# Performance work log

Measured on AMD Instinct MI355X. Metric: run time of the kernel, lower is better.

Reference implementation:

```python
import jax, jax.numpy as jnp
import numpy as np
from jax import lax

SIM_RATIO = 0.5
TAU = 1e-4
BN_EPS = 1e-5
COS_EPS = 1e-6
LEAKY_SLOPE = 0.01


def setup_inputs() -> dict:
    key = jax.random.key(0)
    ks = jax.random.split(key, 4)
    B, N, D = 2048, 50000, 128
    user_item_id = jax.random.randint(ks[0], (B, 2), 0, N, dtype=jnp.int64 if jax.config.jax_enable_x64 else jnp.int32).astype(jnp.int32)
    item_feature = jax.random.normal(ks[1], (B, 2 * D), dtype=jnp.float32)
    all_items = jax.random.normal(ks[2], (N, D), dtype=jnp.float32)
    # Linear(2D -> D) params (stored transposed: x @ W + b), BatchNorm1d affine params
    W = jax.random.normal(ks[3], (2 * D, D), dtype=jnp.float32) / np.float32(np.sqrt(2 * D))
    b = jnp.zeros((D,), jnp.float32)
    gamma = jnp.ones((D,), jnp.float32)
    beta = jnp.zeros((D,), jnp.float32)
    return {"user_item_id": user_item_id, "item_feature": item_feature,
            "all_items": all_items, "W": W, "b": b, "gamma": gamma, "beta": beta}


def _mlp(x, W, b, gamma, beta):
    # Linear + BatchNorm1d (training mode: batch stats, biased var) + LeakyReLU
    h = x @ W + b                                  # [B, D]
    mean = h.mean(axis=0)
    var = ((h - mean) ** 2).mean(axis=0)
    h = (h - mean) * lax.rsqrt(var + BN_EPS) * gamma + beta
    return jnp.where(h >= 0, h, LEAKY_SLOPE * h)


def reference(user_item_id, item_feature, all_items, W, b, gamma, beta):
    B = item_feature.shape[0]
    N = all_items.shape[0]
    h = _mlp(item_feature, W, b, gamma, beta)       # [B, D]
    scores = h @ all_items.T                         # [B, N]
    # hard gumbel-softmax, tau=1e-4
    g = jax.random.gumbel(jax.random.key(42), scores.shape, scores.dtype)
    soft = jax.nn.softmax((scores + g) / TAU, axis=-1)
    idx = jnp.argmax(soft, axis=-1)                  # [B]
    onehot = jax.nn.one_hot(idx, N, dtype=scores.dtype)
    probs = onehot + soft - lax.stop_gradient(soft)  # straight-through hard one-hot
    repl_feat = probs @ all_items                    # [B, D] (one-hot gather via matmul)
    repl_items = (jnp.arange(N, dtype=scores.dtype) * probs).sum(axis=1).astype(jnp.int32)
    orig_feat = all_items[user_item_id[:, 1]]        # [B, D]
    # cosine similarity along dim=1 with eps=1e-6 (torch semantics)
    dot = (orig_feat * repl_feat).sum(axis=1)
    n1 = jnp.maximum(jnp.linalg.norm(orig_feat, axis=1), COS_EPS)
    n2 = jnp.maximum(jnp.linalg.norm(repl_feat, axis=1), COS_EPS)
    sim = dot / (n1 * n2)
    sim = (sim + 1.0) / 2.0                          # regularize_similarity
    labels = jnp.full((B,), SIM_RATIO, dtype=sim.dtype)
    sim_loss = jnp.mean((sim - labels) ** 2)         # SimilarityMarginLoss ~ MSE to ratio
    return repl_items, sim_loss, sim.mean()
```

## Files before the change

### kernel.cpp

```cpp
#include <hip/hip_runtime.h>
#include <math.h>

#define TINYF 1.17549435e-38f
#define GMAX 16.0f
#define NT16 3125
#define SPT16 49

typedef __attribute__((ext_vector_type(8))) short bf16x8;
typedef __attribute__((ext_vector_type(4))) float f32x4;

__device__ __forceinline__ unsigned rotl32(unsigned x, int r) {
  return (x << r) | (x >> (32 - r));
}

__device__ __forceinline__ unsigned tf2x32_xor(unsigned x0, unsigned x1) {
  const unsigned k0 = 0u, k1 = 42u, k2 = 0x1BD11BF0u;
  x0 += k0; x1 += k1;
#define TFR(r) { x0 += x1; x1 = rotl32(x1, r); x1 ^= x0; }
  TFR(13) TFR(15) TFR(26) TFR(6)
  x0 += k1; x1 += k2 + 1u;
  TFR(17) TFR(29) TFR(16) TFR(24)
  x0 += k2; x1 += k0 + 2u;
  TFR(13) TFR(15) TFR(26) TFR(6)
  x0 += k0; x1 += k1 + 3u;
  TFR(17) TFR(29) TFR(16) TFR(24)
  x0 += k1; x1 += k2 + 4u;
  TFR(13) TFR(15) TFR(26) TFR(6)
  x0 += k2; x1 += k0 + 5u;
#undef TFR
  return x0 ^ x1;
}

__device__ __forceinline__ float gumbel_from_bits(unsigned bits) {
  float f = __uint_as_float((bits >> 9) | 0x3f800000u) - 1.0f;
  float u = fmaxf(f, TINYF);
  return -logf(-logf(u));
}

__device__ __forceinline__ unsigned ordf(float v) {
  unsigned b = __float_as_uint(v);
  return (b & 0x80000000u) ? ~b : (b | 0x80000000u);
}
__device__ __forceinline__ float unordf(unsigned u) {
  unsigned b = (u & 0x80000000u) ? (u & 0x7FFFFFFFu) : ~u;
  return __uint_as_float(b);
}

__device__ __forceinline__ unsigned short f2bf(float f) {
  unsigned u = __float_as_uint(f);
  unsigned r = u + 0x7FFFu + ((u >> 16) & 1u);
  return (unsigned short)(r >> 16);
}
__device__ __forceinline__ unsigned pk2(float a, float b) {
  return (unsigned)f2bf(a) | ((unsigned)f2bf(b) << 16);
}
__device__ __forceinline__ int bswz(int b) { return b ^ (((b >> 8) & 7) << 4); }

__device__ __attribute__((noinline)) void resolve_cand(
    int R, int J, float s, float ERRC,
    const float* __restrict__ hfin, const float* __restrict__ items,
    const unsigned* __restrict__ V0u,
    unsigned long long* __restrict__ rowslot, const volatile unsigned* hiw) {
  const unsigned v0 = V0u[R];
  const unsigned hi0 = hiw[2 * R + 1];
  float tv = v0 ? unordf(v0) : -3.4e38f;
  if (hi0) tv = fmaxf(tv, unordf(hi0));
  const float thr2 = tv - ERRC;
  const float d = thr2 - s;
  const unsigned bits = tf2x32_xor(0u, (unsigned)R * 50000u + (unsigned)J);
  const float f = __uint_as_float((bits >> 9) | 0x3f800000u) - 1.0f;
  const float u = fmaxf(f, TINYF);
  const float thr_u = __expf(-__expf(-d)) * (1.0f - 2e-5f);
  if (u < thr_u) return;
  const float g = -logf(-logf(u));
  if (s + g < thr2) return;
  const float4* hp = (const float4*)(hfin + (size_t)R * 128);
  const float4* ap = (const float4*)(items + (size_t)J * 128);
  float4 a4 = {0.f, 0.f, 0.f, 0.f};
#pragma unroll
  for (int k = 0; k < 32; ++k) {
    float4 h = hp[k];
    float4 b = ap[k];
    a4.x = fmaf(h.x, b.x, a4.x);
    a4.y = fmaf(h.y, b.y, a4.y);
    a4.z = fmaf(h.z, b.z, a4.z);
    a4.w = fmaf(h.w, b.w, a4.w);
  }
  const float v = ((a4.x + a4.y) + (a4.z + a4.w)) + g;
  const unsigned ov = ordf(v);
  if (ov >= hiw[2 * R + 1]) {
    const unsigned long long pk =
        ((unsigned long long)ov << 32) | (0xFFFFFFFFu - (unsigned)J);
    atomicMax(&rowslot[R], pk);
  }
}

__global__ void k_hraw(const float* __restrict__ x, const float* __restrict__ W,
                       const float* __restrict__ b, float* __restrict__ hraw,
                       unsigned long long* __restrict__ rowslot,
                       unsigned* __restrict__ V0u, float* __restrict__ norms) {
  __shared__ float sx[256];
  const int i = blockIdx.x;
  const int d = threadIdx.x;
  if (d == 0) {
    rowslot[i] = 0ull;
    V0u[i] = 0u;
    if (i == 0) { norms[0] = 0.0f; norms[1] = 0.0f; }
  }
  sx[d] = x[i * 256 + d];
  sx[d + 128] = x[i * 256 + 128 + d];
  __syncthreads();
  double acc = 0.0;
  for (int k = 0; k < 256; ++k)
    acc = fma((double)sx[k], (double)W[k * 128 + d], acc);
  hraw[i * 128 + d] = (float)acc + b[d];
}

__global__ void k_bca(const float* __restrict__ items,
                      unsigned short* __restrict__ ib,
                      float* __restrict__ norms) {
  __shared__ float red[4];
  const int t = threadIdx.x;
  const int row = blockIdx.x * 32 + (t >> 3);
  const int rc = row > 49999 ? 49999 : row;
  const int c = (t & 7) * 16;
  const float4* p = (const float4*)(items + (size_t)rc * 128 + c);
  const float4 v0 = p[0], v1 = p[1], v2 = p[2], v3 = p[3];
  float ss = v0.x * v0.x + v0.y * v0.y + v0.z * v0.z + v0.w * v0.w +
             v1.x * v1.x + v1.y * v1.y + v1.z * v1.z + v1.w * v1.w +
             v2.x * v2.x + v2.y * v2.y + v2.z * v2.z + v2.w * v2.w +
             v3.x * v3.x + v3.y * v3.y + v3.z * v3.z + v3.w * v3.w;
  if (row <= 49999) {
    uint4 o0, o1;
    o0.x = pk2(v0.x, v0.y); o0.y = pk2(v0.z, v0.w);
    o0.z = pk2(v1.x, v1.y); o0.w = pk2(v1.z, v1.w);
    o1.x = pk2(v2.x, v2.y); o1.y = pk2(v2.z, v2.w);
    o1.z = pk2(v3.x, v3.y); o1.w = pk2(v3.z, v3.w);
    uint4* dst = (uint4*)(ib + (size_t)row * 128 + c);
    dst[0] = o0; dst[1] = o1;
  }
  ss += __shfl_xor(ss, 1);
  ss += __shfl_xor(ss, 2);
  ss += __shfl_xor(ss, 4);
  ss = fmaxf(ss, __shfl_xor(ss, 8));
  ss = fmaxf(ss, __shfl_xor(ss, 16));
  ss = fmaxf(ss, __shfl_xor(ss, 32));
  if ((t & 63) == 0) red[t >> 6] = ss;
  __syncthreads();
  if (t == 0) {
    float mx = fmaxf(fmaxf(red[0], red[1]), fmaxf(red[2], red[3]));
    atomicMax((unsigned*)&norms[1], __float_as_uint(mx));
  }
}

__global__ void k_bnstats(const float* __restrict__ hraw,
                          float* __restrict__ meanv, float* __restrict__ rsv) {
  __shared__ double red[256];
  const int d = blockIdx.x;
  const int t = threadIdx.x;
  double s = 0.0;
  for (int i = t; i < 2048; i += 256) s += (double)hraw[i * 128 + d];
  red[t] = s;
  __syncthreads();
  for (int off = 128; off > 0; off >>= 1) {
    if (t < off) red[t] += red[t + off];
    __syncthreads();
  }
  const float m = (float)(red[0] * (1.0 / 2048.0));
  __syncthreads();
  double v = 0.0;
  for (int i = t; i < 2048; i += 256) {
    float dd = __fsub_rn(hraw[i * 128 + d], m);
    v += (double)dd * (double)dd;
  }
  red[t] = v;
  __syncthreads();
  for (int off = 128; off > 0; off >>= 1) {
    if (t < off) red[t] += red[t + off];
    __syncthreads();
  }
  if (t == 0) {
    float var = (float)(red[0] * (1.0 / 2048.0));
    float vpe = __fadd_rn(var, 1e-5f);
    meanv[d] = m;
    rsv[d] = (float)(1.0 / sqrt((double)vpe));
  }
}

__global__ void k_apply(const float* __restrict__ hraw,
                        const float* __restrict__ meanv, const float* __restrict__ rsv,
                        const float* __restrict__ gamma, const float* __restrict__ beta,
                        float* __restrict__ hfin, unsigned short* __restrict__ hb,
                        float* __restrict__ norms) {
  __shared__ float red[256];
  const int t = threadIdx.x;
  const int idx = blockIdx.x * 256 + t;
  const int d = idx & 127;
  float h = hraw[idx];
  float hn = __fadd_rn(__fmul_rn(__fmul_rn(__fsub_rn(h, meanv[d]), rsv[d]), gamma[d]), beta[d]);
  float o = (hn >= 0.0f) ? hn : __fmul_rn(0.01f, hn);
  hfin[idx] = o;
  hb[idx] = f2bf(o);
  red[t] = o * o;
  __syncthreads();
  for (int off = 64; off > 0; off >>= 1) {
    if ((t & 127) < off) red[t] += red[t + off];
    __syncthreads();
  }
  if ((t & 127) == 0) atomicMax((unsigned*)&norms[0], __float_as_uint(red[t]));
}

__global__ __launch_bounds__(256, 2) void k_seed(
    const unsigned short* __restrict__ hb, const unsigned short* __restrict__ ib,
    const float* __restrict__ norms, unsigned* __restrict__ V0u) {
  const int t = threadIdx.x;
  const int w = t >> 6, l = t & 63;
  const int lg = l >> 4, lr = l & 15;
  const int rg = blockIdx.x >> 3;
  const int jspan = blockIdx.x & 7;
  const int r0w = rg * 64 + w * 16;
  const float ERRC = 0.004f * sqrtf(norms[0] * norms[1]) + 0.01f;

  const unsigned short* aB0 = hb + (size_t)(r0w + lr) * 128 + lg * 8;
  bf16x8 Afrag[4];
#pragma unroll
  for (int kb = 0; kb < 4; ++kb) Afrag[kb] = *(const bf16x8*)(aB0 + kb * 32);

  float vmax[4] = {-3.4e38f, -3.4e38f, -3.4e38f, -3.4e38f};
  for (int itr = 0; itr < 8; ++itr) {
    const int J = jspan * 128 + itr * 16 + lr;
    const unsigned short* bp = ib + (size_t)J * 128 + lg * 8;
    f32x4 acc = (f32x4){0.f, 0.f, 0.f, 0.f};
#pragma unroll
    for (int kb = 0; kb < 4; ++kb)
      acc = __builtin_amdgcn_mfma_f32_16x16x32_bf16(Afrag[kb], *(const bf16x8*)(bp + kb * 32), acc, 0, 0, 0);
#pragma unroll
    for (int q = 0; q < 4; ++q) {
      const int R = r0w + lg * 4 + q;
      const float g = gumbel_from_bits(tf2x32_xor(0u, (unsigned)R * 50000u + (unsigned)J));
      vmax[q] = fmaxf(vmax[q], acc[q] + g);
    }
  }
#pragma unroll
  for (int m = 1; m <= 8; m <<= 1)
#pragma unroll
    for (int q = 0; q < 4; ++q) vmax[q] = fmaxf(vmax[q], __shfl_xor(vmax[q], m));
  if (lr == 0) {
#pragma unroll
    for (int q = 0; q < 4; ++q)
      atomicMax(&V0u[r0w + lg * 4 + q], ordf(vmax[q] - ERRC));
  }
}

__global__ __launch_bounds__(256, 2) void k_screen(
    const unsigned short* __restrict__ hb, const float* __restrict__ hfin,
    const float* __restrict__ items, const unsigned short* __restrict__ ib,
    const unsigned* __restrict__ V0u,
    const float* __restrict__ norms, unsigned long long* __restrict__ rowslot) {
  __shared__ __align__(16) unsigned short Bs[4][2][16 * 128];
  __shared__ unsigned qk[4][128];
  __shared__ float qsh[4][128];

  const int t = threadIdx.x;
  const int w = t >> 6, l = t & 63;
  const int lg = l >> 4, lr = l & 15;
  const int rg = blockIdx.x >> 6;
  const int span = blockIdx.x & 63;
  const int r0w = rg * 64 + w * 16;
  const int tile0 = span * SPT16;
  int nt = NT16 - tile0;
  nt = nt < 0 ? 0 : (nt > SPT16 ? SPT16 : nt);
  if (nt == 0) return;

  const float ERRC = 0.004f * sqrtf(norms[0] * norms[1]) + 0.01f;
  const volatile unsigned* hiw = (const volatile unsigned*)rowslot;

  const unsigned short* aB0 = hb + (size_t)(r0w + lr) * 128 + lg * 8;
  bf16x8 Afrag[4];
#pragma unroll
  for (int kb = 0; kb < 4; ++kb) Afrag[kb] = *(const bf16x8*)(aB0 + kb * 32);

  char* wlds = (char*)Bs + w * 8192;
  const char* ibc = (const char*)ib;
  int so[4];
#pragma unroll
  for (int c = 0; c < 4; ++c) {
    const int row = c * 4 + (l >> 4);
    const int col = (l & 15) * 16;
    so[c] = row * 256 + (col ^ ((row & 7) << 4));
  }

#define ISSUE(tl, pbuf)                                                        \
  {                                                                            \
    const char* gs = ibc + (size_t)(tl) * 4096;                                \
    char* ld = wlds + (pbuf) * 4096;                                           \
    __builtin_amdgcn_global_load_lds((const unsigned*)(gs + so[0]),            \
                                     (unsigned*)(ld), 16, 0, 0);               \
    __builtin_amdgcn_global_load_lds((const unsigned*)(gs + so[1]),            \
                                     (unsigned*)(ld + 1024), 16, 0, 0);        \
    __builtin_amdgcn_global_load_lds((const unsigned*)(gs + so[2]),            \
                                     (unsigned*)(ld + 2048), 16, 0, 0);        \
    __builtin_amdgcn_global_load_lds((const unsigned*)(gs + so[3]),            \
                                     (unsigned*)(ld + 3072), 16, 0, 0);        \
  }
#define WAITVM4() { asm volatile("s_waitcnt vmcnt(4)" ::: "memory"); \
                    __builtin_amdgcn_sched_barrier(0); }
#define WAITVM0() { asm volatile("s_waitcnt vmcnt(0)" ::: "memory"); \
                    __builtin_amdgcn_sched_barrier(0); }

  ISSUE(tile0, 0)

  const unsigned long long lml = (1ull << l) - 1ull;
  unsigned qn = 0;
  float th1[4];

  int pb = 0;
  for (int it = 0; it < nt; ++it) {
    const int j0 = (tile0 + it) * 16;

    if (it + 1 < nt) {
      ISSUE(tile0 + it + 1, pb ^ 1)
      WAITVM4()
    } else {
      WAITVM0()
    }

    if ((it & 7) == 0) {
      float tvl = -3.4e38f;
      if (l < 16) {
        const int R = r0w + l;
        const unsigned v0 = V0u[R];
        if (v0) tvl = unordf(v0);
        const unsigned hi = hiw[2 * R + 1];
        if (hi) tvl = fmaxf(tvl, unordf(hi));
      }
#pragma unroll
      for (int q = 0; q < 4; ++q)
        th1[q] = __shfl(tvl, lg * 4 + q) - GMAX - ERRC;
    }

    f32x4 a0 = (f32x4){0.f, 0.f, 0.f, 0.f};
    f32x4 a1 = (f32x4){0.f, 0.f, 0.f, 0.f};
    const char* tb = wlds + pb * 4096;
    {
      bf16x8 b0 = *(const bf16x8*)(tb + bswz(lr * 256 + 0 * 64 + lg * 16));
      bf16x8 b1 = *(const bf16x8*)(tb + bswz(lr * 256 + 1 * 64 + lg * 16));
      bf16x8 b2 = *(const bf16x8*)(tb + bswz(lr * 256 + 2 * 64 + lg * 16));
      bf16x8 b3 = *(const bf16x8*)(tb + bswz(lr * 256 + 3 * 64 + lg * 16));
      a0 = __builtin_amdgcn_mfma_f32_16x16x32_bf16(Afrag[0], b0, a0, 0, 0, 0);
      a1 = __builtin_amdgcn_mfma_f32_16x16x32_bf16(Afrag[1], b1, a1, 0, 0, 0);
      a0 = __builtin_amdgcn_mfma_f32_16x16x32_bf16(Afrag[2], b2, a0, 0, 0, 0);
      a1 = __builtin_amdgcn_mfma_f32_16x16x32_bf16(Afrag[3], b3, a1, 0, 0, 0);
    }
    const f32x4 acc = a0 + a1;

#pragma unroll
    for (int q = 0; q < 4; ++q) {
      const float s = acc[q];
      const int J = j0 + lr;
      const bool c = (s >= th1[q]);
      const unsigned long long m = __ballot(c);
      if (m) {
        if (c) {
          const unsigned idx = qn + (unsigned)__popcll(m & lml);
          qk[w][idx] = ((unsigned)(lg * 4 + q) << 16) | (unsigned)J;
          qsh[w][idx] = s;
        }
        qn += (unsigned)__popcll(m);
        if (qn >= 64) {
          for (unsigned i = (unsigned)l; i < qn; i += 64) {
            const unsigned key = qk[w][i];
            resolve_cand(r0w + (int)(key >> 16), (int)(key & 0xFFFFu),
                         qsh[w][i], ERRC, hfin, items, V0u, rowslot, hiw);
          }
          qn = 0;
        }
      }
    }

    pb ^= 1;
  }

  for (unsigned i = (unsigned)l; i < qn; i += 64) {
    const unsigned key = qk[w][i];
    resolve_cand(r0w + (int)(key >> 16), (int)(key & 0xFFFFu),
                 qsh[w][i], ERRC, hfin, items, V0u, rowslot, hiw);
  }
#undef ISSUE
#undef WAITVM4
#undef WAITVM0
}

__global__ void k_final(const unsigned long long* __restrict__ rowslot,
                        const int* __restrict__ uid, const float* __restrict__ items,
                        float* __restrict__ dout, float* __restrict__ simv) {
  const int r = blockIdx.x;
  const int lane = threadIdx.x;
  const unsigned long long pk = rowslot[r];
  const int bi = (int)(0xFFFFFFFFu - (unsigned)pk);
  if (lane == 0) dout[r] = (float)bi;

  const int orig = uid[r * 2 + 1];
  float o1 = items[(size_t)orig * 128 + lane];
  float o2 = items[(size_t)orig * 128 + 64 + lane];
  float p1 = items[(size_t)bi * 128 + lane];
  float p2 = items[(size_t)bi * 128 + 64 + lane];
  float d = o1 * p1 + o2 * p2;
  float s1 = o1 * o1 + o2 * o2;
  float s2 = p1 * p1 + p2 * p2;
  for (int off = 32; off > 0; off >>= 1) {
    d += __shfl_down(d, off);
    s1 += __shfl_down(s1, off);
    s2 += __shfl_down(s2, off);
  }
  if (lane == 0) {
    float n1 = fmaxf(sqrtf(s1), 1e-6f);
    float n2 = fmaxf(sqrtf(s2), 1e-6f);
    float sim = d / (n1 * n2);
    simv[r] = (sim + 1.0f) * 0.5f;
  }
}

__global__ void k_reduce(const float* __restrict__ simv, float* __restrict__ dout) {
  __shared__ double rl[256];
  __shared__ double rs[256];
  const int t = threadIdx.x;
  double L = 0.0, S = 0.0;
  for (int i = t; i < 2048; i += 256) {
    double s = (double)simv[i];
    double dd = s - 0.5;
    L += dd * dd;
    S += s;
  }
  rl[t] = L; rs[t] = S;
  __syncthreads();
  for (int off = 128; off > 0; off >>= 1) {
    if (t < off) { rl[t] += rl[t + off]; rs[t] += rs[t + off]; }
    __syncthreads();
  }
  if (t == 0) {
    dout[2048] = (float)(rl[0] * (1.0 / 2048.0));
    dout[2049] = (float)(rs[0] * (1.0 / 2048.0));
  }
}

extern "C" void kernel_launch(void* const* d_in, const int* in_sizes, int n_in,
                              void* d_out, int out_size, void* d_ws, size_t ws_size,
                              hipStream_t stream) {
  const int* uid = (const int*)d_in[0];
  const float* xfeat = (const float*)d_in[1];
  const float* items = (const float*)d_in[2];
  const float* W = (const float*)d_in[3];
  const float* bias = (const float*)d_in[4];
  const float* gamma = (const float*)d_in[5];
  const float* beta = (const float*)d_in[6];

  float* ws = (float*)d_ws;
  float* hraw = ws;
  float* hfin = ws + 262144;
  float* meanv = ws + 524288;
  float* rsv = ws + 524416;
  unsigned* V0u = (unsigned*)(ws + 524544);
  float* simv = ws + 526592;
  float* norms = ws + 528640;
  unsigned long long* rowslot =
      (unsigned long long*)(ws + 528642);
  unsigned short* hb = (unsigned short*)(ws + 532740);
  unsigned short* ib = (unsigned short*)(ws + 663812);
  float* dout = (float*)d_out;

  hipLaunchKernelGGL(k_hraw, dim3(2048), dim3(128), 0, stream, xfeat, W, bias, hraw, rowslot, V0u, norms);
  hipLaunchKernelGGL(k_bca, dim3(1563), dim3(256), 0, stream, items, ib, norms);
  hipLaunchKernelGGL(k_bnstats, dim3(128), dim3(256), 0, stream, hraw, meanv, rsv);
  hipLaunchKernelGGL(k_apply, dim3(1024), dim3(256), 0, stream, hraw, meanv, rsv, gamma, beta, hfin, hb, norms);
  hipLaunchKernelGGL(k_seed, dim3(256), dim3(256), 0, stream, hb, ib, norms, V0u);
  hipLaunchKernelGGL(k_screen, dim3(2048), dim3(256), 0, stream, hb, hfin, items, ib, V0u, norms, rowslot);
  hipLaunchKernelGGL(k_final, dim3(2048), dim3(64), 0, stream, rowslot, uid, items, dout, simv);
  hipLaunchKernelGGL(k_reduce, dim3(1), dim3(256), 0, stream, simv, dout);
}
```

Measured before the change: 356.4 us.

## Process two row tiles per wave in screen kernel and fuse pre-kernels

Each wave in the screening kernel now covers 32 rows (two 16-row A fragments) instead of 16. Every loaded B tile of item embeddings feeds twice as many MFMAs, which halves the grid and the repeated item-tile traffic. The hraw linear and bf16 conversion kernels are merged into a single launch, and the per-row init is replaced with memsets. The trade-off is higher register pressure from the doubled fragments and accumulators, and fewer blocks to balance the screening work.

```diff
diff --git a/kernel.cpp b/kernel.cpp
--- a/kernel.cpp
+++ b/kernel.cpp
@@ -95,61 +95,56 @@
   }
 }
 
-__global__ void k_hraw(const float* __restrict__ x, const float* __restrict__ W,
-                       const float* __restrict__ b, float* __restrict__ hraw,
-                       unsigned long long* __restrict__ rowslot,
-                       unsigned* __restrict__ V0u, float* __restrict__ norms) {
-  __shared__ float sx[256];
-  const int i = blockIdx.x;
-  const int d = threadIdx.x;
-  if (d == 0) {
-    rowslot[i] = 0ull;
-    V0u[i] = 0u;
-    if (i == 0) { norms[0] = 0.0f; norms[1] = 0.0f; }
-  }
-  sx[d] = x[i * 256 + d];
-  sx[d + 128] = x[i * 256 + 128 + d];
-  __syncthreads();
-  double acc = 0.0;
-  for (int k = 0; k < 256; ++k)
-    acc = fma((double)sx[k], (double)W[k * 128 + d], acc);
-  hraw[i * 128 + d] = (float)acc + b[d];
-}
-
-__global__ void k_bca(const float* __restrict__ items,
-                      unsigned short* __restrict__ ib,
-                      float* __restrict__ norms) {
+__global__ void k_pre(const float* __restrict__ x, const float* __restrict__ W,
+                      const float* __restrict__ b, float* __restrict__ hraw,
+                      const float* __restrict__ items,
+                      unsigned short* __restrict__ ib, float* __restrict__ norms) {
+  __shared__ float sx[2][256];
   __shared__ float red[4];
   const int t = threadIdx.x;
-  const int row = blockIdx.x * 32 + (t >> 3);
-  const int rc = row > 49999 ? 49999 : row;
-  const int c = (t & 7) * 16;
-  const float4* p = (const float4*)(items + (size_t)rc * 128 + c);
-  const float4 v0 = p[0], v1 = p[1], v2 = p[2], v3 = p[3];
-  float ss = v0.x * v0.x + v0.y * v0.y + v0.z * v0.z + v0.w * v0.w +
-             v1.x * v1.x + v1.y * v1.y + v1.z * v1.z + v1.w * v1.w +
-             v2.x * v2.x + v2.y * v2.y + v2.z * v2.z + v2.w * v2.w +
-             v3.x * v3.x + v3.y * v3.y + v3.z * v3.z + v3.w * v3.w;
-  if (row <= 49999) {
-    uint4 o0, o1;
-    o0.x = pk2(v0.x, v0.y); o0.y = pk2(v0.z, v0.w);
-    o0.z = pk2(v1.x, v1.y); o0.w = pk2(v1.z, v1.w);
-    o1.x = pk2(v2.x, v2.y); o1.y = pk2(v2.z, v2.w);
-    o1.z = pk2(v3.x, v3.y); o1.w = pk2(v3.z, v3.w);
-    uint4* dst = (uint4*)(ib + (size_t)row * 128 + c);
-    dst[0] = o0; dst[1] = o1;
-  }
-  ss += __shfl_xor(ss, 1);
-  ss += __shfl_xor(ss, 2);
-  ss += __shfl_xor(ss, 4);
-  ss = fmaxf(ss, __shfl_xor(ss, 8));
-  ss = fmaxf(ss, __shfl_xor(ss, 16));
-  ss = fmaxf(ss, __shfl_xor(ss, 32));
-  if ((t & 63) == 0) red[t >> 6] = ss;
-  __syncthreads();
-  if (t == 0) {
-    float mx = fmaxf(fmaxf(red[0], red[1]), fmaxf(red[2], red[3]));
-    atomicMax((unsigned*)&norms[1], __float_as_uint(mx));
+  const int bid = blockIdx.x;
+  if (bid < 1024) {
+    const int rr = t >> 7, d = t & 127;
+    const int i = bid * 2 + rr;
+    sx[rr][d] = x[i * 256 + d];
+    sx[rr][d + 128] = x[i * 256 + 128 + d];
+    __syncthreads();
+    double acc = 0.0;
+    for (int k = 0; k < 256; ++k)
+      acc = fma((double)sx[rr][k], (double)W[k * 128 + d], acc);
+    hraw[i * 128 + d] = (float)acc + b[d];
+  } else {
+    const int bb = bid - 1024;
+    const int row = bb * 32 + (t >> 3);
+    const int rc = row > 49999 ? 49999 : row;
+    const int c = (t & 7) * 16;
+    const float4* p = (const float4*)(items + (size_t)rc * 128 + c);
+    const float4 v0 = p[0], v1 = p[1], v2 = p[2], v3 = p[3];
+    float ss = v0.x * v0.x + v0.y * v0.y + v0.z * v0.z + v0.w * v0.w +
+               v1.x * v1.x + v1.y * v1.y + v1.z * v1.z + v1.w * v1.w +
+               v2.x * v2.x + v2.y * v2.y + v2.z * v2.z + v2.w * v2.w +
+               v3.x * v3.x + v3.y * v3.y + v3.z * v3.z + v3.w * v3.w;
+    if (row <= 49999) {
+      uint4 o0, o1;
+      o0.x = pk2(v0.x, v0.y); o0.y = pk2(v0.z, v0.w);
+      o0.z = pk2(v1.x, v1.y); o0.w = pk2(v1.z, v1.w);
+      o1.x = pk2(v2.x, v2.y); o1.y = pk2(v2.z, v2.w);
+      o1.z = pk2(v3.x, v3.y); o1.w = pk2(v3.z, v3.w);
+      uint4* dst = (uint4*)(ib + (size_t)row * 128 + c);
+      dst[0] = o0; dst[1] = o1;
+    }
+    ss += __shfl_xor(ss, 1);
+    ss += __shfl_xor(ss, 2);
+    ss += __shfl_xor(ss, 4);
+    ss = fmaxf(ss, __shfl_xor(ss, 8));
+    ss = fmaxf(ss, __shfl_xor(ss, 16));
+    ss = fmaxf(ss, __shfl_xor(ss, 32));
+    if ((t & 63) == 0) red[t >> 6] = ss;
+    __syncthreads();
+    if (t == 0) {
+      float mx = fmaxf(fmaxf(red[0], red[1]), fmaxf(red[2], red[3]));
+      atomicMax((unsigned*)&norms[1], __float_as_uint(mx));
+    }
   }
 }
 
@@ -266,7 +261,7 @@
   const int lg = l >> 4, lr = l & 15;
   const int rg = blockIdx.x >> 6;
   const int span = blockIdx.x & 63;
-  const int r0w = rg * 64 + w * 16;
+  const int r0w = rg * 128 + w * 32;
   const int tile0 = span * SPT16;
   int nt = NT16 - tile0;
   nt = nt < 0 ? 0 : (nt > SPT16 ? SPT16 : nt);
@@ -276,9 +271,12 @@
   const volatile unsigned* hiw = (const volatile unsigned*)rowslot;
 
   const unsigned short* aB0 = hb + (size_t)(r0w + lr) * 128 + lg * 8;
-  bf16x8 Afrag[4];
-#pragma unroll
-  for (int kb = 0; kb < 4; ++kb) Afrag[kb] = *(const bf16x8*)(aB0 + kb * 32);
+  bf16x8 Afrag[2][4];
+#pragma unroll
+  for (int kb = 0; kb < 4; ++kb) {
+    Afrag[0][kb] = *(const bf16x8*)(aB0 + kb * 32);
+    Afrag[1][kb] = *(const bf16x8*)(aB0 + 16 * 128 + kb * 32);
+  }
 
   char* wlds = (char*)Bs + w * 8192;
   const char* ibc = (const char*)ib;
@@ -312,7 +310,7 @@
 
   const unsigned long long lml = (1ull << l) - 1ull;
   unsigned qn = 0;
-  float th1[4];
+  float th1[2][4];
 
   int pb = 0;
   for (int it = 0; it < nt; ++it) {
@@ -327,7 +325,7 @@
 
     if ((it & 7) == 0) {
       float tvl = -3.4e38f;
-      if (l < 16) {
+      if (l < 32) {
         const int R = r0w + l;
         const unsigned v0 = V0u[R];
         if (v0) tvl = unordf(v0);
@@ -335,48 +333,59 @@
         if (hi) tvl = fmaxf(tvl, unordf(hi));
       }
 #pragma unroll
-      for (int q = 0; q < 4; ++q)
-        th1[q] = __shfl(tvl, lg * 4 + q) - GMAX - ERRC;
-    }
-
-    f32x4 a0 = (f32x4){0.f, 0.f, 0.f, 0.f};
-    f32x4 a1 = (f32x4){0.f, 0.f, 0.f, 0.f};
+      for (int rt = 0; rt < 2; ++rt)
+#pragma unroll
+        for (int q = 0; q < 4; ++q)
+          th1[rt][q] = __shfl(tvl, rt * 16 + lg * 4 + q) - GMAX - ERRC;
+    }
+
+    f32x4 p0 = (f32x4){0.f, 0.f, 0.f, 0.f};
+    f32x4 p1 = (f32x4){0.f, 0.f, 0.f, 0.f};
+    f32x4 q0 = (f32x4){0.f, 0.f, 0.f, 0.f};
+    f32x4 q1 = (f32x4){0.f, 0.f, 0.f, 0.f};
     const char* tb = wlds + pb * 4096;
     {
       bf16x8 b0 = *(const bf16x8*)(tb + bswz(lr * 256 + 0 * 64 + lg * 16));
       bf16x8 b1 = *(const bf16x8*)(tb + bswz(lr * 256 + 1 * 64 + lg * 16));
       bf16x8 b2 = *(const bf16x8*)(tb + bswz(lr * 256 + 2 * 64 + lg * 16));
       bf16x8 b3 = *(const bf16x8*)(tb + bswz(lr * 256 + 3 * 64 + lg * 16));
-      a0 = __builtin_amdgcn_mfma_f32_16x16x32_bf16(Afrag[0], b0, a0, 0, 0, 0);
-      a1 = __builtin_amdgcn_mfma_f32_16x16x32_bf16(Afrag[1], b1, a1, 0, 0, 0);
-      a0 = __builtin_amdgcn_mfma_f32_16x16x32_bf16(Afrag[2], b2, a0, 0, 0, 0);
-      a1 = __builtin_amdgcn_mfma_f32_16x16x32_bf16(Afrag[3], b3, a1, 0, 0, 0);
-    }
-    const f32x4 acc = a0 + a1;
-
-#pragma unroll
-    for (int q = 0; q < 4; ++q) {
-      const float s = acc[q];
-      const int J = j0 + lr;
-      const bool c = (s >= th1[q]);
-      const unsigned long long m = __ballot(c);
-      if (m) {
-        if (c) {
-          const unsigned idx = qn + (unsigned)__popcll(m & lml);
-          qk[w][idx] = ((unsigned)(lg * 4 + q) << 16) | (unsigned)J;
-          qsh[w][idx] = s;
-        }
-        qn += (unsigned)__popcll(m);
-        if (qn >= 64) {
-          for (unsigned i = (unsigned)l; i < qn; i += 64) {
-            const unsigned key = qk[w][i];
-            resolve_cand(r0w + (int)(key >> 16), (int)(key & 0xFFFFu),
-                         qsh[w][i], ERRC, hfin, items, V0u, rowslot, hiw);
+      p0 = __builtin_amdgcn_mfma_f32_16x16x32_bf16(Afrag[0][0], b0, p0, 0, 0, 0);
+      q0 = __builtin_amdgcn_mfma_f32_16x16x32_bf16(Afrag[1][0], b0, q0, 0, 0, 0);
+      p1 = __builtin_amdgcn_mfma_f32_16x16x32_bf16(Afrag[0][1], b1, p1, 0, 0, 0);
+      q1 = __builtin_amdgcn_mfma_f32_16x16x32_bf16(Afrag[1][1], b1, q1, 0, 0, 0);
+      p0 = __builtin_amdgcn_mfma_f32_16x16x32_bf16(Afrag[0][2], b2, p0, 0, 0, 0);
+      q0 = __builtin_amdgcn_mfma_f32_16x16x32_bf16(Afrag[1][2], b2, q0, 0, 0, 0);
+      p1 = __builtin_amdgcn_mfma_f32_16x16x32_bf16(Afrag[0][3], b3, p1, 0, 0, 0);
+      q1 = __builtin_amdgcn_mfma_f32_16x16x32_bf16(Afrag[1][3], b3, q1, 0, 0, 0);
+    }
+    const f32x4 acc0 = p0 + p1;
+    const f32x4 acc1 = q0 + q1;
+
+#pragma unroll
+    for (int rt = 0; rt < 2; ++rt)
+#pragma unroll
+      for (int q = 0; q < 4; ++q) {
+        const float s = rt ? acc1[q] : acc0[q];
+        const int J = j0 + lr;
+        const bool c = (s >= th1[rt][q]);
+        const unsigned long long m = __ballot(c);
+        if (m) {
+          if (c) {
+            const unsigned idx = qn + (unsigned)__popcll(m & lml);
+            qk[w][idx] = ((unsigned)(rt * 16 + lg * 4 + q) << 16) | (unsigned)J;
+            qsh[w][idx] = s;
           }
-          qn = 0;
+          qn += (unsigned)__popcll(m);
+          if (qn >= 64) {
+            for (unsigned i = (unsigned)l; i < qn; i += 64) {
+              const unsigned key = qk[w][i];
+              resolve_cand(r0w + (int)(key >> 16), (int)(key & 0xFFFFu),
+                           qsh[w][i], ERRC, hfin, items, V0u, rowslot, hiw);
+            }
+            qn = 0;
+          }
         }
       }
-    }
 
     pb ^= 1;
   }
@@ -469,12 +478,14 @@
   unsigned short* ib = (unsigned short*)(ws + 663812);
   float* dout = (float*)d_out;
 
-  hipLaunchKernelGGL(k_hraw, dim3(2048), dim3(128), 0, stream, xfeat, W, bias, hraw, rowslot, V0u, norms);
-  hipLaunchKernelGGL(k_bca, dim3(1563), dim3(256), 0, stream, items, ib, norms);
+  hipMemsetAsync(V0u, 0, 2048 * 4, stream);
+  hipMemsetAsync(norms, 0, 8 + 2048 * 8, stream);
+
+  hipLaunchKernelGGL(k_pre, dim3(2587), dim3(256), 0, stream, xfeat, W, bias, hraw, items, ib, norms);
   hipLaunchKernelGGL(k_bnstats, dim3(128), dim3(256), 0, stream, hraw, meanv, rsv);
   hipLaunchKernelGGL(k_apply, dim3(1024), dim3(256), 0, stream, hraw, meanv, rsv, gamma, beta, hfin, hb, norms);
   hipLaunchKernelGGL(k_seed, dim3(256), dim3(256), 0, stream, hb, ib, norms, V0u);
-  hipLaunchKernelGGL(k_screen, dim3(2048), dim3(256), 0, stream, hb, hfin, items, ib, V0u, norms, rowslot);
+  hipLaunchKernelGGL(k_screen, dim3(1024), dim3(256), 0, stream, hb, hfin, items, ib, V0u, norms, rowslot);
   hipLaunchKernelGGL(k_final, dim3(2048), dim3(64), 0, stream, rowslot, uid, items, dout, simv);
   hipLaunchKernelGGL(k_reduce, dim3(1), dim3(256), 0, stream, simv, dout);
 }
```

Result: faster. 335.9 us (-5.7%).
